# Kernel tuning notes

Hardware: AMD Instinct MI355X
Metric: run time of the kernel (lower is better)

## Reference

```python
import jax, jax.numpy as jnp
import numpy as np

RADIUS = 0.1
KSIZE = 3          # kernel points per dimension
P_DIM = 3
K = KSIZE ** P_DIM  # 27 kernel points
KP_EXTENT = RADIUS / (KSIZE - 1) * P_DIM ** 0.5


def _kernel_points():
    # grid kernel points, same as getKernelPoints(radius, 3, dim=3)
    xyz = np.linspace(-1.0, 1.0, KSIZE)
    pts = np.meshgrid(*P_DIM * [xyz])
    pts = np.vstack([p.flatten() for p in pts]).T
    pts = pts / P_DIM ** 0.5
    return jnp.asarray(pts * RADIUS, dtype=jnp.float32)  # [K, 3]


def setup_inputs() -> dict:
    key = jax.random.key(0)
    k1, k2, k3, k4, k5 = jax.random.split(key, 5)
    N, S, H, CIN, COUT = 40000, 40000, 32, 64, 64
    # points in a [0, 0.2]^3 cube so neighbor offsets are comparable to radius
    q_pts = jax.random.uniform(k1, (N, 3), jnp.float32) * 0.2
    s_pts = jax.random.uniform(k2, (S, 3), jnp.float32) * 0.2
    neighb_inds = jax.random.randint(k3, (N, H), 0, S)
    x = jax.random.normal(k4, (S, CIN), jnp.float32)
    # kaiming-style init for the [K, Cin, Cout] grouped weights
    weights = jax.random.normal(k5, (K, CIN, COUT), jnp.float32) * (1.0 / np.sqrt(CIN))
    return {"q_pts": q_pts, "s_pts": s_pts, "neighb_inds": neighb_inds,
            "x": x, "weights": weights}


def reference(q_pts, s_pts, neighb_inds, x, weights):
    kp = _kernel_points()  # [K, 3], non-trainable constant
    # shadow padding row (sentinel point far away, zero feature)
    s_pad = jnp.concatenate([s_pts, jnp.full((1, s_pts.shape[-1]), 1e6, s_pts.dtype)], axis=0)
    x_pad = jnp.concatenate([x, jnp.zeros((1, x.shape[-1]), x.dtype)], axis=0)
    neighbors = s_pad[neighb_inds] - q_pts[:, None, :]      # [N, H, 3]
    neighb_x = x_pad[neighb_inds]                           # [N, H, Cin]
    # kernel-point influence weights: linear correlation clipped at 0
    diff = neighbors[:, :, None, :] - kp[None, None, :, :]  # [N, H, K, 3]
    sq_dist = jnp.sum(diff * diff, axis=-1)                 # [N, H, K]
    all_w = jnp.maximum(1.0 - jnp.sqrt(sq_dist) / KP_EXTENT, 0.0)
    # weighted grouped matmul over K kernel weight matrices
    fx = jnp.einsum('nhl,nhi,lio->no', all_w, neighb_x, weights)  # [N, Cout]
    return fx
```

## Files before the change

### kernel.cpp

```cpp
#include <hip/hip_runtime.h>

typedef _Float16 half_t;
typedef __fp16   fp16x2 __attribute__((ext_vector_type(2)));
typedef _Float16 half4_t __attribute__((ext_vector_type(4)));
typedef _Float16 half8   __attribute__((ext_vector_type(8)));
typedef float    f32x4   __attribute__((ext_vector_type(4)));
typedef unsigned short u16x8 __attribute__((ext_vector_type(8)));

#define KP_S    0.057735026918962574f
#define INV_EXT 11.547005383792515f
#define GPITCH  3616
#define NBLK    512
#define NTILE   2500

union H8 { half8 v; fp16x2 h2[4]; };
union H4 { half4_t v; fp16x2 h2[2]; };

__global__ void build_wt(const float* __restrict__ W, half_t* __restrict__ WT) {
    int t = blockIdx.x * 256 + threadIdx.x;
    if (t >= 64 * 1792) return;
    int o = t / 1792, k = t - o * 1792;
    int i = k / 28,   l = k - i * 28;
    int c = 4 * (i & 15) + (i >> 4);
    WT[t] = (l < 27) ? (half_t)W[(l * 64 + c) * 64 + o] : (half_t)0.f;
}

#define ISSUE_XV1(BUF, Q, XV) do {                                             \
    u16x8 id8 = *(const u16x8*)&idx_lds[BUF][Q][8 * g];                        \
    _Pragma("unroll")                                                          \
    for (int j = 0; j < 8; ++j)                                                \
        XV[j] = *(const f32x4*)(x + (int)id8[j] * 64 + 4 * lr);                \
} while (0)

#define PACK_B(XV, BF) do {                                                    \
    _Pragma("unroll")                                                          \
    for (int nt = 0; nt < 4; ++nt) {                                           \
        _Pragma("unroll")                                                      \
        for (int p = 0; p < 4; ++p)                                            \
            BF[nt].h2[p] = __builtin_amdgcn_cvt_pkrtz(XV[2 * p][nt],           \
                                                      XV[2 * p + 1][nt]);      \
    }                                                                          \
} while (0)

#define MFMA_DUMP(Q, CUR, BF) do {                                             \
    float w0v[8], w1v[8];                                                      \
    _Pragma("unroll")                                                          \
    for (int j = 0; j < 8; ++j) {                                              \
        f32x4 nb = nbr_lds[CUR][Q][8 * g + j];                                 \
        float dx = nb.x - kx0, dy = nb.y - ky0, dz = nb.z - kz0;               \
        w0v[j] = fmaxf(fmaf(__builtin_amdgcn_sqrtf(dx*dx + dy*dy + dz*dz), -INV_EXT, 1.f), 0.f); \
        float ex = nb.x - kx1, ey = nb.y - ky1, ez = nb.z - kz1;               \
        w1v[j] = fmaxf(fmaf(__builtin_amdgcn_sqrtf(ex*ex + ey*ey + ez*ez), -INV_EXT, cbias), 0.f); \
    }                                                                          \
    H8 A0, A1;                                                                 \
    _Pragma("unroll")                                                          \
    for (int p = 0; p < 4; ++p) {                                              \
        A0.h2[p] = __builtin_amdgcn_cvt_pkrtz(w0v[2*p], w0v[2*p+1]);           \
        A1.h2[p] = __builtin_amdgcn_cvt_pkrtz(w1v[2*p], w1v[2*p+1]);           \
    }                                                                          \
    char* gq = g_mem + (Q) * GPITCH;                                           \
    _Pragma("unroll")                                                          \
    for (int nt = 0; nt < 4; ++nt) {                                           \
        f32x4 z = {0.f, 0.f, 0.f, 0.f};                                        \
        f32x4 c0 = __builtin_amdgcn_mfma_f32_16x16x32_f16(A0.v, BF[nt].v, z, 0, 0, 0); \
        f32x4 c1 = __builtin_amdgcn_mfma_f32_16x16x32_f16(A1.v, BF[nt].v, z, 0, 0, 0); \
        const int ic = 16 * nt + lr;                                           \
        H4 h0;                                                                 \
        h0.h2[0] = __builtin_amdgcn_cvt_pkrtz(c0[0], c0[1]);                   \
        h0.h2[1] = __builtin_amdgcn_cvt_pkrtz(c0[2], c0[3]);                   \
        *(half4_t*)(gq + 2 * (ic * 28 + 4 * g)) = h0.v;                        \
        if (4 * g < 12) {                                                      \
            H4 h1;                                                             \
            h1.h2[0] = __builtin_amdgcn_cvt_pkrtz(c1[0], c1[1]);               \
            h1.h2[1] = __builtin_amdgcn_cvt_pkrtz(c1[2], c1[3]);               \
            *(half4_t*)(gq + 2 * (ic * 28 + 16 + 4 * g)) = h1.v;               \
        }                                                                      \
    }                                                                          \
} while (0)

#define BODY(T, TN, CUR, XV) do {                                              \
              \
    f32x4 xvB[8];                                                              \
    ISSUE_XV1(CUR, 2 * wid + 1, xvB);                                          \
    H8 BFA[4];                                                                 \
    PACK_B(XV, BFA);                                                           \
    const int nn   = (TN) * 16 + aq;                                           \
    const int idxN = inds[nn * 32 + ah];                                       \
    MFMA_DUMP(2 * wid, CUR, BFA);                                              \
    f32x4 vN;                                                                  \
    vN.x = s_pts[idxN * 3 + 0] - q_pts[nn * 3 + 0];                            \
    vN.y = s_pts[idxN * 3 + 1] - q_pts[nn * 3 + 1];                            \
    vN.z = s_pts[idxN * 3 + 2] - q_pts[nn * 3 + 2];                            \
    vN.w = 0.f;                                                                \
    H8 BFB[4];                                                                 \
    PACK_B(xvB, BFB);                                                          \
    MFMA_DUMP(2 * wid + 1, CUR, BFB);                                          \
    idx_lds[(CUR) ^ 1][aq][ah] = (unsigned short)idxN;                         \
    nbr_lds[(CUR) ^ 1][aq][ah] = vN;                                           \
    __syncthreads();                                                           \
                              \
    ISSUE_XV1((CUR) ^ 1, 2 * wid, XV);                                         \
             \
    const half_t* wrow = WT + (16 * ot + lr) * 1792 + kh * 896 + 8 * g;        \
    const char*   gb   = g_mem + lr * GPITCH + kh * 1792;                      \
    f32x4 accA = {0.f, 0.f, 0.f, 0.f}, accB = {0.f, 0.f, 0.f, 0.f};            \
    _Pragma("unroll 7")                                                        \
    for (int s = 0; s < 28; s += 2) {                                          \
        half8 aA = *(const half8*)(gb + 64 * s + 16 * g);                      \
        half8 bA = *(const half8*)(wrow + 32 * s);                             \
        accA = __builtin_amdgcn_mfma_f32_16x16x32_f16(aA, bA, accA, 0, 0, 0);  \
        half8 aB = *(const half8*)(gb + 64 * (s + 1) + 16 * g);                \
        half8 bB = *(const half8*)(wrow + 32 * (s + 1));                       \
        accB = __builtin_amdgcn_mfma_f32_16x16x32_f16(aB, bB, accB, 0, 0, 0);  \
    }                                                                          \
    f32x4 acc = accA + accB;                                                   \
    if (kh) *(f32x4*)&red[ot][lane] = acc;                                     \
    __syncthreads();                                                           \
    if (!kh) {                                                                 \
        f32x4 p = red[ot][lane];                                               \
        const int o = 16 * ot + lr;                                            \
        _Pragma("unroll")                                                      \
        for (int r = 0; r < 4; ++r)                                            \
            out[((T) * 16 + 4 * g + r) * 64 + o] = acc[r] + p[r];              \
    }                                                                          \
} while (0)

__global__ __launch_bounds__(512, 4) void kpconv(
    const float* __restrict__ q_pts, const float* __restrict__ s_pts,
    const int*   __restrict__ inds,  const float* __restrict__ x,
    const half_t* __restrict__ WT,   float* __restrict__ out)
{
    __shared__ __align__(16) char   g_mem[16 * GPITCH];
    __shared__ __align__(16) unsigned short idx_lds[2][16][32];
    __shared__ __align__(16) f32x4  nbr_lds[2][16][32];
    __shared__ __align__(16) f32x4  red[4][64];

    const int tid  = threadIdx.x;
    const int lane = tid & 63, wid = tid >> 6;
    const int lr   = lane & 15, g = lane >> 4;
    const int aq   = tid >> 5,  ah = tid & 31;
    const int ot   = wid & 3,   kh = wid >> 2;

    const float kx0 = (float)((lr / 3) % 3 - 1) * KP_S;
    const float ky0 = (float)( lr / 9      - 1) * KP_S;
    const float kz0 = (float)( lr % 3      - 1) * KP_S;
    const int   l1  = lr + 16;
    const float kx1 = (float)((l1 / 3) % 3 - 1) * KP_S;
    const float ky1 = (float)( l1 / 9      - 1) * KP_S;
    const float kz1 = (float)( l1 % 3      - 1) * KP_S;
    const float cbias = (l1 < 27) ? 1.f : -1.f;

    {
        int n   = blockIdx.x * 16 + aq;
        int idx = inds[n * 32 + ah];
        idx_lds[0][aq][ah] = (unsigned short)idx;
        f32x4 v;
        v.x = s_pts[idx * 3 + 0] - q_pts[n * 3 + 0];
        v.y = s_pts[idx * 3 + 1] - q_pts[n * 3 + 1];
        v.z = s_pts[idx * 3 + 2] - q_pts[n * 3 + 2];
        v.w = 0.f;
        nbr_lds[0][aq][ah] = v;
    }
    __syncthreads();

    f32x4 xv[8];
    ISSUE_XV1(0, 2 * wid, xv);

    int cur = 0;
    for (int t = blockIdx.x; t < NTILE; t += NBLK) {
        int tn = (t + NBLK < NTILE) ? t + NBLK : t;
        BODY(t, tn, cur, xv);
        cur ^= 1;
    }
}

extern "C" void kernel_launch(void* const* d_in, const int* in_sizes, int n_in,
                              void* d_out, int out_size, void* d_ws, size_t ws_size,
                              hipStream_t stream) {
    const float* q_pts = (const float*)d_in[0];
    const float* s_pts = (const float*)d_in[1];
    const int*   inds  = (const int*)d_in[2];
    const float* x     = (const float*)d_in[3];
    const float* W     = (const float*)d_in[4];
    float* out = (float*)d_out;
    half_t* WT = (half_t*)d_ws;

    build_wt<<<448, 256, 0, stream>>>(W, WT);
    kpconv<<<NBLK, 512, 0, stream>>>(q_pts, s_pts, inds, x, WT, out);
}
```

Measured before the change: 100.2 us.

## Double tile to 32 queries per 1024-thread block with swizzled LDS and 4-way K split

```diff
diff --git a/kernel.cpp b/kernel.cpp
--- a/kernel.cpp
+++ b/kernel.cpp
@@ -9,9 +9,9 @@
 
 #define KP_S    0.057735026918962574f
 #define INV_EXT 11.547005383792515f
-#define GPITCH  3616
-#define NBLK    512
-#define NTILE   2500
+#define GPITCH  3584
+#define NBLK    256
+#define NTILE   1250
 
 union H8 { half8 v; fp16x2 h2[4]; };
 union H4 { half4_t v; fp16x2 h2[2]; };
@@ -29,7 +29,8 @@
     u16x8 id8 = *(const u16x8*)&idx_lds[BUF][Q][8 * g];                        \
     _Pragma("unroll")                                                          \
     for (int j = 0; j < 8; ++j)                                                \
-        XV[j] = *(const f32x4*)(x + (int)id8[j] * 64 + 4 * lr);                \
+        XV[j] = __builtin_nontemporal_load(                                    \
+                    (const f32x4*)(x + (int)id8[j] * 64 + 4 * lr));            \
 } while (0)
 
 #define PACK_B(XV, BF) do {                                                    \
@@ -46,10 +47,11 @@
     float w0v[8], w1v[8];                                                      \
     _Pragma("unroll")                                                          \
     for (int j = 0; j < 8; ++j) {                                              \
-        f32x4 nb = nbr_lds[CUR][Q][8 * g + j];                                 \
-        float dx = nb.x - kx0, dy = nb.y - ky0, dz = nb.z - kz0;               \
+        half4_t nb = nbr_lds[CUR][Q][8 * g + j];                               \
+        float nx = (float)nb[0], ny = (float)nb[1], nz = (float)nb[2];         \
+        float dx = nx - kx0, dy = ny - ky0, dz = nz - kz0;                     \
         w0v[j] = fmaxf(fmaf(__builtin_amdgcn_sqrtf(dx*dx + dy*dy + dz*dz), -INV_EXT, 1.f), 0.f); \
-        float ex = nb.x - kx1, ey = nb.y - ky1, ez = nb.z - kz1;               \
+        float ex = nx - kx1, ey = ny - ky1, ez = nz - kz1;                     \
         w1v[j] = fmaxf(fmaf(__builtin_amdgcn_sqrtf(ex*ex + ey*ey + ez*ez), -INV_EXT, cbias), 0.f); \
     }                                                                          \
     H8 A0, A1;                                                                 \
@@ -59,6 +61,7 @@
         A1.h2[p] = __builtin_amdgcn_cvt_pkrtz(w1v[2*p], w1v[2*p+1]);           \
     }                                                                          \
     char* gq = g_mem + (Q) * GPITCH;                                           \
+    const int xq = ((Q) & 7) << 4;                                             \
     _Pragma("unroll")                                                          \
     for (int nt = 0; nt < 4; ++nt) {                                           \
         f32x4 z = {0.f, 0.f, 0.f, 0.f};                                        \
@@ -68,72 +71,80 @@
         H4 h0;                                                                 \
         h0.h2[0] = __builtin_amdgcn_cvt_pkrtz(c0[0], c0[1]);                   \
         h0.h2[1] = __builtin_amdgcn_cvt_pkrtz(c0[2], c0[3]);                   \
-        *(half4_t*)(gq + 2 * (ic * 28 + 4 * g)) = h0.v;                        \
+        *(half4_t*)(gq + ((2 * (ic * 28 + 4 * g)) ^ xq)) = h0.v;               \
         if (4 * g < 12) {                                                      \
             H4 h1;                                                             \
             h1.h2[0] = __builtin_amdgcn_cvt_pkrtz(c1[0], c1[1]);               \
             h1.h2[1] = __builtin_amdgcn_cvt_pkrtz(c1[2], c1[3]);               \
-            *(half4_t*)(gq + 2 * (ic * 28 + 16 + 4 * g)) = h1.v;               \
+            *(half4_t*)(gq + ((2 * (ic * 28 + 16 + 4 * g)) ^ xq)) = h1.v;      \
         }                                                                      \
     }                                                                          \
 } while (0)
 
-#define BODY(T, TN, CUR, XV) do {                                              \
-              \
+#define BODY(T, TN, CUR) do {                                                  \
+                    \
     f32x4 xvB[8];                                                              \
     ISSUE_XV1(CUR, 2 * wid + 1, xvB);                                          \
+                     \
+    const int nn   = (TN) * 32 + aq;                                           \
+    const int idxN = inds[nn * 32 + ah];                                       \
+    const float sx = s_pts[idxN * 3 + 0] - q_pts[nn * 3 + 0];                  \
+    const float sy = s_pts[idxN * 3 + 1] - q_pts[nn * 3 + 1];                  \
+    const float sz = s_pts[idxN * 3 + 2] - q_pts[nn * 3 + 2];                  \
+                                              \
     H8 BFA[4];                                                                 \
-    PACK_B(XV, BFA);                                                           \
-    const int nn   = (TN) * 16 + aq;                                           \
-    const int idxN = inds[nn * 32 + ah];                                       \
+    PACK_B(xv, BFA);                                                           \
     MFMA_DUMP(2 * wid, CUR, BFA);                                              \
-    f32x4 vN;                                                                  \
-    vN.x = s_pts[idxN * 3 + 0] - q_pts[nn * 3 + 0];                            \
-    vN.y = s_pts[idxN * 3 + 1] - q_pts[nn * 3 + 1];                            \
-    vN.z = s_pts[idxN * 3 + 2] - q_pts[nn * 3 + 2];                            \
-    vN.w = 0.f;                                                                \
     H8 BFB[4];                                                                 \
     PACK_B(xvB, BFB);                                                          \
     MFMA_DUMP(2 * wid + 1, CUR, BFB);                                          \
     idx_lds[(CUR) ^ 1][aq][ah] = (unsigned short)idxN;                         \
-    nbr_lds[(CUR) ^ 1][aq][ah] = vN;                                           \
+    { H4 nv;                                                                   \
+      nv.h2[0] = __builtin_amdgcn_cvt_pkrtz(sx, sy);                           \
+      nv.h2[1] = __builtin_amdgcn_cvt_pkrtz(sz, 0.f);                          \
+      nbr_lds[(CUR) ^ 1][aq][ah] = nv.v; }                                     \
     __syncthreads();                                                           \
-                              \
-    ISSUE_XV1((CUR) ^ 1, 2 * wid, XV);                                         \
-             \
-    const half_t* wrow = WT + (16 * ot + lr) * 1792 + kh * 896 + 8 * g;        \
-    const char*   gb   = g_mem + lr * GPITCH + kh * 1792;                      \
-    f32x4 accA = {0.f, 0.f, 0.f, 0.f}, accB = {0.f, 0.f, 0.f, 0.f};            \
-    _Pragma("unroll 7")                                                        \
-    for (int s = 0; s < 28; s += 2) {                                          \
-        half8 aA = *(const half8*)(gb + 64 * s + 16 * g);                      \
+                             \
+    ISSUE_XV1((CUR) ^ 1, 2 * wid, xv);                                         \
+                             \
+    const half_t* wrow = WT + (16 * ot + lr) * 1792 + kh * 448 + 8 * g;        \
+    const char* gb0 = g_mem + lr * GPITCH;                                     \
+    const char* gb1 = g_mem + (16 + lr) * GPITCH;                              \
+    const int koff = 896 * kh + 16 * g;                                        \
+    const int xr   = (lr & 7) << 4;                                            \
+    f32x4 acc0 = {0.f, 0.f, 0.f, 0.f}, acc1 = {0.f, 0.f, 0.f, 0.f};            \
+    _Pragma("unroll")                                                          \
+    for (int s = 0; s < 14; ++s) {                                             \
         half8 bA = *(const half8*)(wrow + 32 * s);                             \
-        accA = __builtin_amdgcn_mfma_f32_16x16x32_f16(aA, bA, accA, 0, 0, 0);  \
-        half8 aB = *(const half8*)(gb + 64 * (s + 1) + 16 * g);                \
-        half8 bB = *(const half8*)(wrow + 32 * (s + 1));                       \
-        accB = __builtin_amdgcn_mfma_f32_16x16x32_f16(aB, bB, accB, 0, 0, 0);  \
-    }                                                                          \
-    f32x4 acc = accA + accB;                                                   \
-    if (kh) *(f32x4*)&red[ot][lane] = acc;                                     \
+        half8 a0 = *(const half8*)(gb0 + ((koff + 64 * s) ^ xr));              \
+        half8 a1 = *(const half8*)(gb1 + ((koff + 64 * s) ^ xr));              \
+        acc0 = __builtin_amdgcn_mfma_f32_16x16x32_f16(a0, bA, acc0, 0, 0, 0);  \
+        acc1 = __builtin_amdgcn_mfma_f32_16x16x32_f16(a1, bA, acc1, 0, 0, 0);  \
+    }                                                                          \
+    if (kh) { red[0][kh - 1][ot][lane] = acc0;                                 \
+              red[1][kh - 1][ot][lane] = acc1; }                               \
     __syncthreads();                                                           \
     if (!kh) {                                                                 \
-        f32x4 p = red[ot][lane];                                               \
+        f32x4 r0 = acc0 + red[0][0][ot][lane] + red[0][1][ot][lane] + red[0][2][ot][lane]; \
+        f32x4 r1 = acc1 + red[1][0][ot][lane] + red[1][1][ot][lane] + red[1][2][ot][lane]; \
         const int o = 16 * ot + lr;                                            \
         _Pragma("unroll")                                                      \
-        for (int r = 0; r < 4; ++r)                                            \
-            out[((T) * 16 + 4 * g + r) * 64 + o] = acc[r] + p[r];              \
-    }                                                                          \
-} while (0)
-
-__global__ __launch_bounds__(512, 4) void kpconv(
+        for (int r = 0; r < 4; ++r) {                                          \
+            out[((T) * 32 + 4 * g + r) * 64 + o]      = r0[r];                 \
+            out[((T) * 32 + 16 + 4 * g + r) * 64 + o] = r1[r];                 \
+        }                                                                      \
+    }                                                                          \
+} while (0)
+
+__global__ __launch_bounds__(1024, 4) void kpconv(
     const float* __restrict__ q_pts, const float* __restrict__ s_pts,
     const int*   __restrict__ inds,  const float* __restrict__ x,
     const half_t* __restrict__ WT,   float* __restrict__ out)
 {
-    __shared__ __align__(16) char   g_mem[16 * GPITCH];
-    __shared__ __align__(16) unsigned short idx_lds[2][16][32];
-    __shared__ __align__(16) f32x4  nbr_lds[2][16][32];
-    __shared__ __align__(16) f32x4  red[4][64];
+    __shared__ __align__(16) char    g_mem[32 * GPITCH];
+    __shared__ __align__(16) unsigned short idx_lds[2][32][32];
+    __shared__ __align__(16) half4_t nbr_lds[2][32][32];
+    __shared__ __align__(16) f32x4   red[2][3][4][64];
 
     const int tid  = threadIdx.x;
     const int lane = tid & 63, wid = tid >> 6;
@@ -151,15 +162,16 @@
     const float cbias = (l1 < 27) ? 1.f : -1.f;
 
     {
-        int n   = blockIdx.x * 16 + aq;
+        int n   = blockIdx.x * 32 + aq;
         int idx = inds[n * 32 + ah];
         idx_lds[0][aq][ah] = (unsigned short)idx;
-        f32x4 v;
-        v.x = s_pts[idx * 3 + 0] - q_pts[n * 3 + 0];
-        v.y = s_pts[idx * 3 + 1] - q_pts[n * 3 + 1];
-        v.z = s_pts[idx * 3 + 2] - q_pts[n * 3 + 2];
-        v.w = 0.f;
-        nbr_lds[0][aq][ah] = v;
+        float dx = s_pts[idx * 3 + 0] - q_pts[n * 3 + 0];
+        float dy = s_pts[idx * 3 + 1] - q_pts[n * 3 + 1];
+        float dz = s_pts[idx * 3 + 2] - q_pts[n * 3 + 2];
+        H4 nv;
+        nv.h2[0] = __builtin_amdgcn_cvt_pkrtz(dx, dy);
+        nv.h2[1] = __builtin_amdgcn_cvt_pkrtz(dz, 0.f);
+        nbr_lds[0][aq][ah] = nv.v;
     }
     __syncthreads();
 
@@ -169,7 +181,7 @@
     int cur = 0;
     for (int t = blockIdx.x; t < NTILE; t += NBLK) {
         int tn = (t + NBLK < NTILE) ? t + NBLK : t;
-        BODY(t, tn, cur, xv);
+        BODY(t, tn, cur);
         cur ^= 1;
     }
 }
@@ -186,5 +198,5 @@
     half_t* WT = (half_t*)d_ws;
 
     build_wt<<<448, 256, 0, stream>>>(W, WT);
-    kpconv<<<NBLK, 512, 0, stream>>>(q_pts, s_pts, inds, x, WT, out);
+    kpconv<<<NBLK, 1024, 0, stream>>>(q_pts, s_pts, inds, x, WT, out);
 }
```

Measured after the change: 146.2 us. 1.46x slower.
